# Performance work log

Measured on AMD Instinct MI355X. Metric: run time of the kernel, lower is better.

## Reference

```python
import jax, jax.numpy as jnp
import numpy as np

B, S, E, H = 2, 2048, 1024, 16
D = E // H

def setup_inputs() -> dict:
    key = jax.random.key(0)
    ks = jax.random.split(key, 5)
    return {
        "hidden_states": jax.random.normal(ks[0], (B, S, E), dtype=jnp.float32),
        "c_attn_w": jax.random.normal(ks[1], (E, 3 * E), dtype=jnp.float32) * 0.02,
        "c_attn_b": jax.random.normal(ks[2], (3 * E,), dtype=jnp.float32) * 0.02,
        "c_proj_w": jax.random.normal(ks[3], (E, E), dtype=jnp.float32) * 0.02,
        "c_proj_b": jax.random.normal(ks[4], (E,), dtype=jnp.float32) * 0.02,
    }

def reference(hidden_states, c_attn_w, c_attn_b, c_proj_w, c_proj_b):
    x = hidden_states                      # [B, S, E]
    b, s, _ = x.shape
    w_q, w_k, w_v = jnp.split(c_attn_w, 3, axis=1)   # each [E, E]
    q_b, k_b, v_b = jnp.split(c_attn_b, 3, axis=0)   # each [E]

    # value projection
    v = x @ w_v + v_b                                        # [B,S,E]
    v = v.reshape(b, s, H, D).transpose(0, 2, 1, 3)          # [B,H,S,D]

    # fused query: ((x Wq + qb) Wk^T + kb)
    q = (x @ w_q + q_b) @ w_k.T + k_b                        # [B,S,E]
    qh = q.reshape(b, s, H, D).transpose(0, 2, 1, 3)         # [B,H,S,D]

    # key side is RAW hidden states split per head
    kh = x.reshape(b, s, H, D).transpose(0, 2, 1, 3)         # [B,H,S,D]

    scale = 1.0 / jnp.float32(D) ** 0.5
    scores = jnp.einsum("bhqd,bhkd->bhqk",
                        qh.astype(jnp.float32),
                        kh.astype(jnp.float32)) * scale       # [B,H,S,S] fp32

    causal = jnp.tril(jnp.ones((s, s), dtype=bool))
    mask_value = jnp.finfo(jnp.float32).min
    scores = jnp.where(causal[None, None], scores, mask_value)

    probs = jax.nn.softmax(scores, axis=-1).astype(v.dtype)  # [B,H,S,S]

    out = jnp.einsum("bhqk,bhkd->bhqd", probs, v)            # [B,H,S,D]
    out = out.transpose(0, 2, 1, 3).reshape(b, s, E)         # [B,S,E]
    out = out @ c_proj_w + c_proj_b
    return out
```

## Files before the change

### kernel.cpp

```cpp
#include <hip/hip_runtime.h>

typedef __attribute__((ext_vector_type(8))) __bf16 bf16x8;
typedef __attribute__((ext_vector_type(4))) __bf16 bf16x4;
typedef __attribute__((ext_vector_type(4))) float f32x4;

typedef __attribute__((address_space(1))) void as1_void;
typedef __attribute__((address_space(3))) void as3_void;

__device__ __forceinline__ void gl_lds16(const void* g, void* l) {
    __builtin_amdgcn_global_load_lds((const as1_void*)g, (as3_void*)l, 16, 0, 0);
}

__device__ __forceinline__ const bf16x8* swz(const __bf16* base, int row, int chunk) {
    return (const bf16x8*)((const char*)base + row * 128 + ((chunk ^ (row & 7)) * 16));
}

#define QSCALE (0.125f * 1.44269504f)

__global__ __launch_bounds__(256) void prep_kernel(
    const float* __restrict__ x, const float* __restrict__ caw,
    const float* __restrict__ cpw,
    __bf16* __restrict__ xb, __bf16* __restrict__ wvt,
    __bf16* __restrict__ wpt, __bf16* __restrict__ wqt,
    __bf16* __restrict__ wkn)
{
    __shared__ float tile[32 * 33];
    int bid = blockIdx.x;
    int tid = threadIdx.x;
    if (bid < 1024) {
        int nt = bid >> 5, kt = bid & 31;
        int tx = tid & 31, ty = tid >> 5;
        int n0 = nt * 32, k0 = kt * 32;
#pragma unroll
        for (int i = 0; i < 4; ++i)
            tile[(ty + i * 8) * 33 + tx] = caw[(long)(k0 + ty + i * 8) * 3072 + 2048 + n0 + tx];
        __syncthreads();
#pragma unroll
        for (int i = 0; i < 4; ++i)
            wvt[(long)(n0 + ty + i * 8) * 1024 + k0 + tx] = (__bf16)tile[tx * 33 + ty + i * 8];
    } else if (bid < 2048) {
        int v = bid - 1024;
        int nt = v >> 5, kt = v & 31;
        int tx = tid & 31, ty = tid >> 5;
        int n0 = nt * 32, k0 = kt * 32;
#pragma unroll
        for (int i = 0; i < 4; ++i)
            tile[(ty + i * 8) * 33 + tx] = cpw[(long)(k0 + ty + i * 8) * 1024 + n0 + tx];
        __syncthreads();
#pragma unroll
        for (int i = 0; i < 4; ++i)
            wpt[(long)(n0 + ty + i * 8) * 1024 + k0 + tx] = (__bf16)tile[tx * 33 + ty + i * 8];
    } else if (bid < 3072) {
        int v = bid - 2048;
        int nt = v >> 5, kt = v & 31;
        int tx = tid & 31, ty = tid >> 5;
        int n0 = nt * 32, k0 = kt * 32;
#pragma unroll
        for (int i = 0; i < 4; ++i)
            tile[(ty + i * 8) * 33 + tx] = caw[(long)(k0 + ty + i * 8) * 3072 + n0 + tx];
        __syncthreads();
#pragma unroll
        for (int i = 0; i < 4; ++i)
            wqt[(long)(n0 + ty + i * 8) * 1024 + k0 + tx] = (__bf16)tile[tx * 33 + ty + i * 8];
    } else if (bid < 4096) {
        int e = (bid - 3072) * 1024 + tid * 4;
        int n = e >> 10, k = e & 1023;
        float4 f = *(const float4*)(caw + (long)n * 3072 + 1024 + k);
        bf16x4 o = {(__bf16)f.x, (__bf16)f.y, (__bf16)f.z, (__bf16)f.w};
        *(bf16x4*)(wkn + e) = o;
    } else {
        long e = (long)(bid - 4096) * 1024 + tid * 4;
        float4 f = *(const float4*)(x + e);
        bf16x4 o = {(__bf16)f.x, (__bf16)f.y, (__bf16)f.z, (__bf16)f.w};
        *(bf16x4*)(xb + e) = o;
    }
}

template <bool BF16OUT, int BN>
__global__ __launch_bounds__(256) void gemm_bt(
    const __bf16* __restrict__ A, int lda,
    const __bf16* __restrict__ B, int ldb,
    const float* __restrict__ bias,
    void* __restrict__ C, int ldc, int K, float oscale)
{
    constexpr int NT = BN / 32;
    __shared__ __bf16 As[128 * 64];
    __shared__ __bf16 Bs[BN * 64];
    const int tid = threadIdx.x;
    const int lane = tid & 63;
    const int wave = tid >> 6;
    const int quad = lane >> 4, l16 = lane & 15;
    const long m0 = (long)blockIdx.y * 128;
    const long n0 = (long)blockIdx.x * BN;
    const int wm = (wave >> 1) * 64, wn = (wave & 1) * (BN / 2);

    f32x4 acc[4][NT] = {};

    for (int k0 = 0; k0 < K; k0 += 64) {
#pragma unroll
        for (int c = tid; c < (128 + BN) * 8; c += 256) {
            int row = c >> 3, cc = (c & 7) ^ (row & 7);
            if (row < 128)
                gl_lds16(A + (m0 + row) * lda + k0 + cc * 8, As + c * 8);
            else
                gl_lds16(B + (n0 + row - 128) * ldb + k0 + cc * 8, Bs + (c - 1024) * 8);
        }
        __syncthreads();
#pragma unroll
        for (int kk = 0; kk < 2; ++kk) {
            bf16x8 af[4], bfr[NT];
#pragma unroll
            for (int i = 0; i < 4; ++i)
                af[i] = *swz(As, wm + i * 16 + l16, kk * 4 + quad);
#pragma unroll
            for (int j = 0; j < NT; ++j)
                bfr[j] = *swz(Bs, wn + j * 16 + l16, kk * 4 + quad);
#pragma unroll
            for (int i = 0; i < 4; ++i)
#pragma unroll
                for (int j = 0; j < NT; ++j)
                    acc[i][j] = __builtin_amdgcn_mfma_f32_16x16x32_bf16(af[i], bfr[j], acc[i][j], 0, 0, 0);
        }
        __syncthreads();
    }
#pragma unroll
    for (int i = 0; i < 4; ++i) {
        long row = m0 + wm + i * 16 + quad * 4;
#pragma unroll
        for (int j = 0; j < NT; ++j) {
            int col = (int)n0 + wn + j * 16 + l16;
            float bb = bias ? bias[col] : 0.f;
#pragma unroll
            for (int r = 0; r < 4; ++r) {
                float v = (acc[i][j][r] + bb) * oscale;
                if (BF16OUT)
                    ((__bf16*)C)[(row + r) * ldc + col] = (__bf16)v;
                else
                    ((float*)C)[(row + r) * ldc + col] = v;
            }
        }
    }
}

__global__ __launch_bounds__(256) void gemm_qv(
    const __bf16* __restrict__ Aq,
    const __bf16* __restrict__ Av,
    const __bf16* __restrict__ B,
    const float* __restrict__ bias,
    __bf16* __restrict__ Qout,
    __bf16* __restrict__ VTout)
{
    __shared__ __bf16 smem[128 * 136];
    __bf16* As = smem;
    __bf16* Bs = smem + 8192;
    const int tid = threadIdx.x;
    const int lane = tid & 63;
    const int wave = tid >> 6;
    const int quad = lane >> 4, l16 = lane & 15;
    const long m0 = (long)blockIdx.y * 128;
    const long n0 = (long)blockIdx.x * 128;
    const int wm = (wave >> 1) * 64, wn = (wave & 1) * 64;
    const __bf16* A = (n0 < 1024) ? Aq : Av;
    const float osc = (n0 < 1024) ? QSCALE : 1.0f;

    f32x4 acc[4][4] = {};

    for (int k0 = 0; k0 < 1024; k0 += 64) {
#pragma unroll
        for (int c = tid; c < 2048; c += 256) {
            int row = c >> 3, cc = (c & 7) ^ (row & 7);
            if (row < 128)
                gl_lds16(A + (m0 + row) * 1024 + k0 + cc * 8, As + c * 8);
            else
                gl_lds16(B + (n0 + row - 128) * 1024 + k0 + cc * 8, Bs + (c - 1024) * 8);
        }
        __syncthreads();
#pragma unroll
        for (int kk = 0; kk < 2; ++kk) {
            bf16x8 af[4], bfr[4];
#pragma unroll
            for (int i = 0; i < 4; ++i)
                af[i] = *swz(As, wm + i * 16 + l16, kk * 4 + quad);
#pragma unroll
            for (int j = 0; j < 4; ++j)
                bfr[j] = *swz(Bs, wn + j * 16 + l16, kk * 4 + quad);
#pragma unroll
            for (int i = 0; i < 4; ++i)
#pragma unroll
                for (int j = 0; j < 4; ++j)
                    acc[i][j] = __builtin_amdgcn_mfma_f32_16x16x32_bf16(af[i], bfr[j], acc[i][j], 0, 0, 0);
        }
        __syncthreads();
    }

    if (n0 < 1024) {
#pragma unroll
        for (int i = 0; i < 4; ++i) {
            long row = m0 + wm + i * 16 + quad * 4;
#pragma unroll
            for (int j = 0; j < 4; ++j) {
                int col = (int)n0 + wn + j * 16 + l16;
                float bb = bias[col];
#pragma unroll
                for (int r = 0; r < 4; ++r)
                    Qout[(row + r) * 1024 + col] = (__bf16)((acc[i][j][r] + bb) * osc);
            }
        }
    } else {
        __syncthreads();
#pragma unroll
        for (int i = 0; i < 4; ++i) {
#pragma unroll
            for (int j = 0; j < 4; ++j) {
                int col = (int)n0 + wn + j * 16 + l16;
                float bb = bias[col];
                bf16x4 v;
#pragma unroll
                for (int r = 0; r < 4; ++r) v[r] = (__bf16)(acc[i][j][r] + bb);
                *(bf16x4*)(smem + (wn + j * 16 + l16) * 136 + wm + i * 16 + quad * 4) = v;
            }
        }
        __syncthreads();
        const int d0 = (int)n0 - 1024;
        const int bb = (int)(m0 >> 11);
        const int sl = (int)(m0 & 2047);
#pragma unroll
        for (int pass = 0; pass < 16; ++pass) {
            int idx = pass * 256 + tid;
            int n = idx >> 5;
            int mc = (idx & 31) * 4;
            bf16x4 v = *(const bf16x4*)(smem + n * 136 + mc);
            *(bf16x4*)(VTout + ((long)(bb * 1024 + d0 + n)) * 2048 + sl + mc) = v;
        }
    }
}

__global__ __launch_bounds__(512) void attn_kernel(
    const __bf16* __restrict__ Q,
    const __bf16* __restrict__ Xb,
    const __bf16* __restrict__ VT,
    __bf16* __restrict__ O)
{
    __shared__ __bf16 Ks[2 * 8192];
    __shared__ __bf16 Vs[2 * 8192];
    __shared__ __bf16 Ps[8 * 1024];
    const int tid = threadIdx.x;
    const int lane = tid & 63;
    const int wave = tid >> 6;
    const int group = wave >> 2;
    const int w4 = wave & 3;
    const int quad = lane >> 4, l16 = lane & 15;
    const int qa = blockIdx.y;
    const int qb = 31 - qa;
    const int qt = group ? qb : qa;
    const int bh = blockIdx.x;
    const int b = bh >> 4, h = bh & 15;
    const long rowbase = (long)b * 2048;

    const int s0 = tid;
    const int c0 = ((s0 & 7) ^ ((s0 >> 3) & 7)) * 8;

    bf16x8 ones;
#pragma unroll
    for (int i = 0; i < 8; ++i) ones[i] = (__bf16)1.0f;

    bf16x8 qfr[2];
    {
        const __bf16* qp = Q + (rowbase + qt * 64 + w4 * 16 + l16) * 1024 + h * 64 + quad * 8;
        qfr[0] = *(const bf16x8*)(qp);
        qfr[1] = *(const bf16x8*)(qp + 32);
    }

    const __bf16* kp0 = Xb + (rowbase + (s0 >> 3)) * 1024 + h * 64 + c0;
    const __bf16* vp0 = VT + ((long)(b * 1024 + h * 64 + (s0 >> 3))) * 2048 + c0;

    auto stage_tile = [&](int j, int buf, int sub) {
        gl_lds16(kp0 + (long)j * 65536, Ks + buf * 8192 + sub * 4096 + s0 * 8);
        gl_lds16(vp0 + j * 64, Vs + buf * 8192 + sub * 4096 + s0 * 8);
    };
    stage_tile(0, 0, 0);
    stage_tile(1, 0, 1);

    const int nouter = (qb + 2) >> 1;

    f32x4 oacc[4] = {};
    f32x4 lacc = {};
    __bf16* Pw = Ps + wave * 1024;

    for (int jj = 0; jj < nouter; ++jj) {
        __syncthreads();
        if (jj + 1 < nouter) {
            stage_tile(2 * jj + 2, (jj + 1) & 1, 0);
            stage_tile(2 * jj + 3, (jj + 1) & 1, 1);
        }

#pragma unroll
        for (int sub = 0; sub < 2; ++sub) {
            const int j = 2 * jj + sub;
            if (j > qt) continue;
            const __bf16* Kb = Ks + (jj & 1) * 8192 + sub * 4096;
            const __bf16* Vb = Vs + (jj & 1) * 8192 + sub * 4096;

            bf16x8 kf[2][4], vf[2][4];
#pragma unroll
            for (int kk = 0; kk < 2; ++kk)
#pragma unroll
                for (int kt = 0; kt < 4; ++kt) {
                    kf[kk][kt] = *swz(Kb, kt * 16 + l16, kk * 4 + quad);
                    vf[kk][kt] = *swz(Vb, kt * 16 + l16, kk * 4 + quad);
                }

            f32x4 sacc[4] = {};
            __builtin_amdgcn_s_setprio(1);
#pragma unroll
            for (int kk = 0; kk < 2; ++kk)
#pragma unroll
                for (int kt = 0; kt < 4; ++kt)
                    sacc[kt] = __builtin_amdgcn_mfma_f32_16x16x32_bf16(
                        kf[kk][kt], qfr[kk], sacc[kt], 0, 0, 0);
            __builtin_amdgcn_s_setprio(0);

            if (j == qt) {
                const int qloc = w4 * 16 + l16;
#pragma unroll
                for (int kt = 0; kt < 4; ++kt) {
                    bf16x4 pk;
#pragma unroll
                    for (int r = 0; r < 4; ++r) {
                        float s = sacc[kt][r];
                        if (kt * 16 + quad * 4 + r > qloc) s = -1e30f;
                        pk[r] = (__bf16)exp2f(s);
                    }
                    *(bf16x4*)((char*)Pw + l16 * 128 +
                               (((kt * 2 + (quad >> 1)) ^ (l16 & 7)) * 16) + (quad & 1) * 8) = pk;
                }
            } else {
#pragma unroll
                for (int kt = 0; kt < 4; ++kt) {
                    bf16x4 pk;
#pragma unroll
                    for (int r = 0; r < 4; ++r)
                        pk[r] = (__bf16)exp2f(sacc[kt][r]);
                    *(bf16x4*)((char*)Pw + l16 * 128 +
                               (((kt * 2 + (quad >> 1)) ^ (l16 & 7)) * 16) + (quad & 1) * 8) = pk;
                }
            }

            __builtin_amdgcn_s_setprio(1);
#pragma unroll
            for (int kk = 0; kk < 2; ++kk) {
                bf16x8 pf = *swz(Pw, l16, kk * 4 + quad);
                lacc = __builtin_amdgcn_mfma_f32_16x16x32_bf16(ones, pf, lacc, 0, 0, 0);
#pragma unroll
                for (int dt = 0; dt < 4; ++dt)
                    oacc[dt] = __builtin_amdgcn_mfma_f32_16x16x32_bf16(
                        vf[kk][dt], pf, oacc[dt], 0, 0, 0);
            }
            __builtin_amdgcn_s_setprio(0);
        }
    }

    {
        float inv = 1.0f / lacc[0];
        long row = rowbase + qt * 64 + w4 * 16 + l16;
#pragma unroll
        for (int dt = 0; dt < 4; ++dt) {
            bf16x4 ov;
#pragma unroll
            for (int r = 0; r < 4; ++r) ov[r] = (__bf16)(oacc[dt][r] * inv);
            *(bf16x4*)(O + row * 1024 + h * 64 + dt * 16 + quad * 4) = ov;
        }
    }
}

extern "C" void kernel_launch(void* const* d_in, const int* in_sizes, int n_in,
                              void* d_out, int out_size, void* d_ws, size_t ws_size,
                              hipStream_t stream) {
    const float* x   = (const float*)d_in[0];
    const float* caw = (const float*)d_in[1];
    const float* cab = (const float*)d_in[2];
    const float* cpw = (const float*)d_in[3];
    const float* cpb = (const float*)d_in[4];

    char* p = (char*)d_ws;
    auto alloc = [&](size_t bytes) {
        void* r = (void*)p;
        p += (bytes + 255) & ~(size_t)255;
        return r;
    };
    __bf16* xb    = (__bf16*)alloc(4096UL * 1024 * 2);
    __bf16* wkn   = (__bf16*)alloc(1024UL * 1024 * 2);
    __bf16* wvt   = (__bf16*)alloc(1024UL * 1024 * 2);
    __bf16* wqt   = (__bf16*)alloc(1024UL * 1024 * 2);
    __bf16* wpt   = (__bf16*)alloc(1024UL * 1024 * 2);
    __bf16* tb    = (__bf16*)alloc(4096UL * 1024 * 2);
    __bf16* qbuf  = (__bf16*)alloc(4096UL * 1024 * 2);
    __bf16* vt    = (__bf16*)alloc(2048UL * 2048 * 2);

    prep_kernel<<<8192, 256, 0, stream>>>(x, caw, cpw, xb, wvt, wpt, wqt, wkn);
    gemm_bt<true, 64><<<dim3(16, 32), 256, 0, stream>>>(xb, 1024, wqt, 1024, cab,
                                                        (void*)tb, 1024, 1024, 1.0f);
    gemm_qv<<<dim3(16, 32), 256, 0, stream>>>(tb, xb, wkn, cab + 1024, qbuf, vt);
    attn_kernel<<<dim3(32, 16), 512, 0, stream>>>(qbuf, xb, vt, tb);
    gemm_bt<false, 64><<<dim3(16, 32), 256, 0, stream>>>(tb, 1024, wpt, 1024, cpb,
                                                         d_out, 1024, 1024, 1.0f);
    (void)in_sizes; (void)n_in; (void)out_size; (void)ws_size;
}
```

Before: 181.2 us.

## Split the long query tile's extra key tiles across both wave groups

In the attention kernel each block pairs a short query tile (qa) with a long one (qb), and the group handling qa used to sit idle once its causal range ended. Key tiles beyond qa are now split between both groups: each group computes half of the 64-key scores and P·V for the qb tile. Group 0's partial output and row sum are combined with group 1's through LDS at the end. This balances work between the two groups at the cost of extra barriers, more registers for a second accumulator set, and a reduction step.

```diff
diff --git a/kernel.cpp b/kernel.cpp
--- a/kernel.cpp
+++ b/kernel.cpp
@@ -161,7 +161,6 @@
     const long n0 = (long)blockIdx.x * 128;
     const int wm = (wave >> 1) * 64, wn = (wave & 1) * 64;
     const __bf16* A = (n0 < 1024) ? Aq : Av;
-    const float osc = (n0 < 1024) ? QSCALE : 1.0f;
 
     f32x4 acc[4][4] = {};
 
@@ -203,7 +202,7 @@
                 float bb = bias[col];
 #pragma unroll
                 for (int r = 0; r < 4; ++r)
-                    Qout[(row + r) * 1024 + col] = (__bf16)((acc[i][j][r] + bb) * osc);
+                    Qout[(row + r) * 1024 + col] = (__bf16)((acc[i][j][r] + bb) * QSCALE);
             }
         }
     } else {
@@ -264,11 +263,14 @@
 #pragma unroll
     for (int i = 0; i < 8; ++i) ones[i] = (__bf16)1.0f;
 
-    bf16x8 qfr[2];
+    bf16x8 qfa[2], qfb[2];
     {
-        const __bf16* qp = Q + (rowbase + qt * 64 + w4 * 16 + l16) * 1024 + h * 64 + quad * 8;
-        qfr[0] = *(const bf16x8*)(qp);
-        qfr[1] = *(const bf16x8*)(qp + 32);
+        const __bf16* qpa = Q + (rowbase + qa * 64 + w4 * 16 + l16) * 1024 + h * 64 + quad * 8;
+        const __bf16* qpb = Q + (rowbase + qb * 64 + w4 * 16 + l16) * 1024 + h * 64 + quad * 8;
+        qfa[0] = *(const bf16x8*)(qpa);
+        qfa[1] = *(const bf16x8*)(qpa + 32);
+        qfb[0] = *(const bf16x8*)(qpb);
+        qfb[1] = *(const bf16x8*)(qpb + 32);
     }
 
     const __bf16* kp0 = Xb + (rowbase + (s0 >> 3)) * 1024 + h * 64 + c0;
@@ -284,8 +286,10 @@
     const int nouter = (qb + 2) >> 1;
 
     f32x4 oacc[4] = {};
-    f32x4 lacc = {};
-    __bf16* Pw = Ps + wave * 1024;
+    f32x4 oacch[4] = {};
+    f32x4 lacc = {}, lacch = {};
+    __bf16* Pown = Ps + wave * 1024;
+    __bf16* Pspl = Ps + w4 * 1024;
 
     for (int jj = 0; jj < nouter; ++jj) {
         __syncthreads();
@@ -297,69 +301,148 @@
 #pragma unroll
         for (int sub = 0; sub < 2; ++sub) {
             const int j = 2 * jj + sub;
-            if (j > qt) continue;
+            if (sub == 1 && 2 * jj == qa) __syncthreads();
+            if (j > qb) continue;
             const __bf16* Kb = Ks + (jj & 1) * 8192 + sub * 4096;
             const __bf16* Vb = Vs + (jj & 1) * 8192 + sub * 4096;
 
-            bf16x8 kf[2][4], vf[2][4];
-#pragma unroll
-            for (int kk = 0; kk < 2; ++kk)
-#pragma unroll
-                for (int kt = 0; kt < 4; ++kt) {
-                    kf[kk][kt] = *swz(Kb, kt * 16 + l16, kk * 4 + quad);
-                    vf[kk][kt] = *swz(Vb, kt * 16 + l16, kk * 4 + quad);
+            if (j <= qa) {
+                bf16x8 kf[2][4], vf[2][4];
+#pragma unroll
+                for (int kk = 0; kk < 2; ++kk)
+#pragma unroll
+                    for (int kt = 0; kt < 4; ++kt) {
+                        kf[kk][kt] = *swz(Kb, kt * 16 + l16, kk * 4 + quad);
+                        vf[kk][kt] = *swz(Vb, kt * 16 + l16, kk * 4 + quad);
+                    }
+
+                f32x4 sacc[4] = {};
+                __builtin_amdgcn_s_setprio(1);
+#pragma unroll
+                for (int kk = 0; kk < 2; ++kk) {
+                    bf16x8 qf = group ? qfb[kk] : qfa[kk];
+#pragma unroll
+                    for (int kt = 0; kt < 4; ++kt)
+                        sacc[kt] = __builtin_amdgcn_mfma_f32_16x16x32_bf16(
+                            kf[kk][kt], qf, sacc[kt], 0, 0, 0);
                 }
-
-            f32x4 sacc[4] = {};
-            __builtin_amdgcn_s_setprio(1);
-#pragma unroll
-            for (int kk = 0; kk < 2; ++kk)
-#pragma unroll
-                for (int kt = 0; kt < 4; ++kt)
-                    sacc[kt] = __builtin_amdgcn_mfma_f32_16x16x32_bf16(
-                        kf[kk][kt], qfr[kk], sacc[kt], 0, 0, 0);
-            __builtin_amdgcn_s_setprio(0);
-
-            if (j == qt) {
+                __builtin_amdgcn_s_setprio(0);
+
+                if (j == qt) {
+                    const int qloc = w4 * 16 + l16;
+#pragma unroll
+                    for (int kt = 0; kt < 4; ++kt) {
+                        bf16x4 pk;
+#pragma unroll
+                        for (int r = 0; r < 4; ++r) {
+                            float s = sacc[kt][r];
+                            if (kt * 16 + quad * 4 + r > qloc) s = -1e30f;
+                            pk[r] = (__bf16)exp2f(s);
+                        }
+                        *(bf16x4*)((char*)Pown + l16 * 128 +
+                                   (((kt * 2 + (quad >> 1)) ^ (l16 & 7)) * 16) + (quad & 1) * 8) = pk;
+                    }
+                } else {
+#pragma unroll
+                    for (int kt = 0; kt < 4; ++kt) {
+                        bf16x4 pk;
+#pragma unroll
+                        for (int r = 0; r < 4; ++r)
+                            pk[r] = (__bf16)exp2f(sacc[kt][r]);
+                        *(bf16x4*)((char*)Pown + l16 * 128 +
+                                   (((kt * 2 + (quad >> 1)) ^ (l16 & 7)) * 16) + (quad & 1) * 8) = pk;
+                    }
+                }
+
+                __builtin_amdgcn_s_setprio(1);
+#pragma unroll
+                for (int kk = 0; kk < 2; ++kk) {
+                    bf16x8 pf = *swz(Pown, l16, kk * 4 + quad);
+                    lacc = __builtin_amdgcn_mfma_f32_16x16x32_bf16(ones, pf, lacc, 0, 0, 0);
+#pragma unroll
+                    for (int dt = 0; dt < 4; ++dt)
+                        oacc[dt] = __builtin_amdgcn_mfma_f32_16x16x32_bf16(
+                            vf[kk][dt], pf, oacc[dt], 0, 0, 0);
+                }
+                __builtin_amdgcn_s_setprio(0);
+            } else {
+                const int ktb = group * 2;
+                bf16x8 kf2[2][2], vf2[4];
+#pragma unroll
+                for (int kk = 0; kk < 2; ++kk)
+#pragma unroll
+                    for (int t = 0; t < 2; ++t)
+                        kf2[kk][t] = *swz(Kb, (ktb + t) * 16 + l16, kk * 4 + quad);
+#pragma unroll
+                for (int dt = 0; dt < 4; ++dt)
+                    vf2[dt] = *swz(Vb, dt * 16 + l16, group * 4 + quad);
+
+                f32x4 s2[2] = {};
+                __builtin_amdgcn_s_setprio(1);
+#pragma unroll
+                for (int kk = 0; kk < 2; ++kk)
+#pragma unroll
+                    for (int t = 0; t < 2; ++t)
+                        s2[t] = __builtin_amdgcn_mfma_f32_16x16x32_bf16(
+                            kf2[kk][t], qfb[kk], s2[t], 0, 0, 0);
+                __builtin_amdgcn_s_setprio(0);
+
                 const int qloc = w4 * 16 + l16;
-#pragma unroll
-                for (int kt = 0; kt < 4; ++kt) {
+                const bool diag = (j == qb);
+#pragma unroll
+                for (int t = 0; t < 2; ++t) {
+                    const int kt = ktb + t;
                     bf16x4 pk;
 #pragma unroll
                     for (int r = 0; r < 4; ++r) {
-                        float s = sacc[kt][r];
-                        if (kt * 16 + quad * 4 + r > qloc) s = -1e30f;
+                        float s = s2[t][r];
+                        if (diag && kt * 16 + quad * 4 + r > qloc) s = -1e30f;
                         pk[r] = (__bf16)exp2f(s);
                     }
-                    *(bf16x4*)((char*)Pw + l16 * 128 +
+                    *(bf16x4*)((char*)Pspl + l16 * 128 +
                                (((kt * 2 + (quad >> 1)) ^ (l16 & 7)) * 16) + (quad & 1) * 8) = pk;
                 }
-            } else {
-#pragma unroll
-                for (int kt = 0; kt < 4; ++kt) {
-                    bf16x4 pk;
-#pragma unroll
-                    for (int r = 0; r < 4; ++r)
-                        pk[r] = (__bf16)exp2f(sacc[kt][r]);
-                    *(bf16x4*)((char*)Pw + l16 * 128 +
-                               (((kt * 2 + (quad >> 1)) ^ (l16 & 7)) * 16) + (quad & 1) * 8) = pk;
+
+                __builtin_amdgcn_s_setprio(1);
+                bf16x8 pf = *swz(Pspl, l16, group * 4 + quad);
+                if (group) {
+                    lacc = __builtin_amdgcn_mfma_f32_16x16x32_bf16(ones, pf, lacc, 0, 0, 0);
+#pragma unroll
+                    for (int dt = 0; dt < 4; ++dt)
+                        oacc[dt] = __builtin_amdgcn_mfma_f32_16x16x32_bf16(
+                            vf2[dt], pf, oacc[dt], 0, 0, 0);
+                } else {
+                    lacch = __builtin_amdgcn_mfma_f32_16x16x32_bf16(ones, pf, lacch, 0, 0, 0);
+#pragma unroll
+                    for (int dt = 0; dt < 4; ++dt)
+                        oacch[dt] = __builtin_amdgcn_mfma_f32_16x16x32_bf16(
+                            vf2[dt], pf, oacch[dt], 0, 0, 0);
                 }
+                __builtin_amdgcn_s_setprio(0);
             }
-
-            __builtin_amdgcn_s_setprio(1);
-#pragma unroll
-            for (int kk = 0; kk < 2; ++kk) {
-                bf16x8 pf = *swz(Pw, l16, kk * 4 + quad);
-                lacc = __builtin_amdgcn_mfma_f32_16x16x32_bf16(ones, pf, lacc, 0, 0, 0);
-#pragma unroll
-                for (int dt = 0; dt < 4; ++dt)
-                    oacc[dt] = __builtin_amdgcn_mfma_f32_16x16x32_bf16(
-                        vf[kk][dt], pf, oacc[dt], 0, 0, 0);
-            }
-            __builtin_amdgcn_s_setprio(0);
-        }
-    }
-
+        }
+    }
+
+    __syncthreads();
+    float* xch = (float*)Ks;
+    if (!group) {
+        const int base = (w4 * 64 + lane) * 20;
+#pragma unroll
+        for (int dt = 0; dt < 4; ++dt)
+            *(f32x4*)(xch + base + dt * 4) = oacch[dt];
+        xch[base + 16] = lacch[0];
+    }
+    __syncthreads();
+    if (group) {
+        const int base = (w4 * 64 + lane) * 20;
+#pragma unroll
+        for (int dt = 0; dt < 4; ++dt) {
+            f32x4 part = *(const f32x4*)(xch + base + dt * 4);
+#pragma unroll
+            for (int r = 0; r < 4; ++r) oacc[dt][r] += part[r];
+        }
+        lacc[0] += xch[base + 16];
+    }
     {
         float inv = 1.0f / lacc[0];
         long row = rowbase + qt * 64 + w4 * 16 + l16;
```

Result: slower. 196.2 us (+8.3%).

## Fuse Q projection into attention kernel and merge T/V projection GEMMs

Applied to the files above, without the earlier changes.

The second-stage Q projection (T·Wk^T) moves into the attention kernel. Each block computes its own 128 Q rows for one head from T and the head's Wk slice, staged through the K/V shared buffers, then places them in registers. The T and V projection GEMMs now share one launch with a flat block index, which removes a kernel launch and the Q buffer round trip through global memory. In exchange the attention kernel does a serial K=1024 GEMM prologue with no overlap. Each T row tile is also reloaded by all 16 heads, and the V GEMM now sits on the critical path alongside T.

```diff
diff --git a/kernel.cpp b/kernel.cpp
--- a/kernel.cpp
+++ b/kernel.cpp
@@ -76,144 +76,110 @@
     }
 }
 
-template <bool BF16OUT, int BN>
-__global__ __launch_bounds__(256) void gemm_bt(
-    const __bf16* __restrict__ A, int lda,
-    const __bf16* __restrict__ B, int ldb,
-    const float* __restrict__ bias,
-    void* __restrict__ C, int ldc, int K, float oscale)
+__global__ __launch_bounds__(256) void gemm_tv(
+    const __bf16* __restrict__ xb, const __bf16* __restrict__ wqt,
+    const __bf16* __restrict__ wvt, const float* __restrict__ cab,
+    __bf16* __restrict__ tb, __bf16* __restrict__ vt)
 {
-    constexpr int NT = BN / 32;
-    __shared__ __bf16 As[128 * 64];
-    __shared__ __bf16 Bs[BN * 64];
+    __shared__ __bf16 smem[128 * 136];
+    const int bid = blockIdx.x;
     const int tid = threadIdx.x;
     const int lane = tid & 63;
     const int wave = tid >> 6;
     const int quad = lane >> 4, l16 = lane & 15;
-    const long m0 = (long)blockIdx.y * 128;
-    const long n0 = (long)blockIdx.x * BN;
-    const int wm = (wave >> 1) * 64, wn = (wave & 1) * (BN / 2);
-
-    f32x4 acc[4][NT] = {};
-
-    for (int k0 = 0; k0 < K; k0 += 64) {
-#pragma unroll
-        for (int c = tid; c < (128 + BN) * 8; c += 256) {
-            int row = c >> 3, cc = (c & 7) ^ (row & 7);
-            if (row < 128)
-                gl_lds16(A + (m0 + row) * lda + k0 + cc * 8, As + c * 8);
-            else
-                gl_lds16(B + (n0 + row - 128) * ldb + k0 + cc * 8, Bs + (c - 1024) * 8);
-        }
-        __syncthreads();
-#pragma unroll
-        for (int kk = 0; kk < 2; ++kk) {
-            bf16x8 af[4], bfr[NT];
-#pragma unroll
-            for (int i = 0; i < 4; ++i)
-                af[i] = *swz(As, wm + i * 16 + l16, kk * 4 + quad);
-#pragma unroll
-            for (int j = 0; j < NT; ++j)
-                bfr[j] = *swz(Bs, wn + j * 16 + l16, kk * 4 + quad);
-#pragma unroll
-            for (int i = 0; i < 4; ++i)
-#pragma unroll
-                for (int j = 0; j < NT; ++j)
-                    acc[i][j] = __builtin_amdgcn_mfma_f32_16x16x32_bf16(af[i], bfr[j], acc[i][j], 0, 0, 0);
-        }
-        __syncthreads();
-    }
-#pragma unroll
-    for (int i = 0; i < 4; ++i) {
-        long row = m0 + wm + i * 16 + quad * 4;
-#pragma unroll
-        for (int j = 0; j < NT; ++j) {
-            int col = (int)n0 + wn + j * 16 + l16;
-            float bb = bias ? bias[col] : 0.f;
-#pragma unroll
-            for (int r = 0; r < 4; ++r) {
-                float v = (acc[i][j][r] + bb) * oscale;
-                if (BF16OUT)
-                    ((__bf16*)C)[(row + r) * ldc + col] = (__bf16)v;
+
+    if (bid < 512) {
+        __bf16* As = smem;
+        __bf16* Bs = smem + 8192;
+        const int bx = bid & 15, by = bid >> 4;
+        const long m0 = (long)by * 128;
+        const long n0 = (long)bx * 64;
+        const int wm = (wave >> 1) * 64, wn = (wave & 1) * 32;
+
+        f32x4 acc[4][2] = {};
+        for (int k0 = 0; k0 < 1024; k0 += 64) {
+#pragma unroll
+            for (int c = tid; c < 1536; c += 256) {
+                int row = c >> 3, cc = (c & 7) ^ (row & 7);
+                if (row < 128)
+                    gl_lds16(xb + (m0 + row) * 1024 + k0 + cc * 8, As + c * 8);
                 else
-                    ((float*)C)[(row + r) * ldc + col] = v;
-            }
-        }
-    }
-}
-
-__global__ __launch_bounds__(256) void gemm_qv(
-    const __bf16* __restrict__ Aq,
-    const __bf16* __restrict__ Av,
-    const __bf16* __restrict__ B,
-    const float* __restrict__ bias,
-    __bf16* __restrict__ Qout,
-    __bf16* __restrict__ VTout)
-{
-    __shared__ __bf16 smem[128 * 136];
-    __bf16* As = smem;
-    __bf16* Bs = smem + 8192;
-    const int tid = threadIdx.x;
-    const int lane = tid & 63;
-    const int wave = tid >> 6;
-    const int quad = lane >> 4, l16 = lane & 15;
-    const long m0 = (long)blockIdx.y * 128;
-    const long n0 = (long)blockIdx.x * 128;
-    const int wm = (wave >> 1) * 64, wn = (wave & 1) * 64;
-    const __bf16* A = (n0 < 1024) ? Aq : Av;
-    const float osc = (n0 < 1024) ? QSCALE : 1.0f;
-
-    f32x4 acc[4][4] = {};
-
-    for (int k0 = 0; k0 < 1024; k0 += 64) {
-#pragma unroll
-        for (int c = tid; c < 2048; c += 256) {
-            int row = c >> 3, cc = (c & 7) ^ (row & 7);
-            if (row < 128)
-                gl_lds16(A + (m0 + row) * 1024 + k0 + cc * 8, As + c * 8);
-            else
-                gl_lds16(B + (n0 + row - 128) * 1024 + k0 + cc * 8, Bs + (c - 1024) * 8);
-        }
-        __syncthreads();
-#pragma unroll
-        for (int kk = 0; kk < 2; ++kk) {
-            bf16x8 af[4], bfr[4];
-#pragma unroll
-            for (int i = 0; i < 4; ++i)
-                af[i] = *swz(As, wm + i * 16 + l16, kk * 4 + quad);
-#pragma unroll
-            for (int j = 0; j < 4; ++j)
-                bfr[j] = *swz(Bs, wn + j * 16 + l16, kk * 4 + quad);
-#pragma unroll
-            for (int i = 0; i < 4; ++i)
-#pragma unroll
-                for (int j = 0; j < 4; ++j)
-                    acc[i][j] = __builtin_amdgcn_mfma_f32_16x16x32_bf16(af[i], bfr[j], acc[i][j], 0, 0, 0);
-        }
-        __syncthreads();
-    }
-
-    if (n0 < 1024) {
+                    gl_lds16(wqt + (n0 + row - 128) * 1024 + k0 + cc * 8, Bs + (c - 1024) * 8);
+            }
+            __syncthreads();
+#pragma unroll
+            for (int kk = 0; kk < 2; ++kk) {
+                bf16x8 af[4], bfr[2];
+#pragma unroll
+                for (int i = 0; i < 4; ++i)
+                    af[i] = *swz(As, wm + i * 16 + l16, kk * 4 + quad);
+#pragma unroll
+                for (int j = 0; j < 2; ++j)
+                    bfr[j] = *swz(Bs, wn + j * 16 + l16, kk * 4 + quad);
+#pragma unroll
+                for (int i = 0; i < 4; ++i)
+#pragma unroll
+                    for (int j = 0; j < 2; ++j)
+                        acc[i][j] = __builtin_amdgcn_mfma_f32_16x16x32_bf16(af[i], bfr[j], acc[i][j], 0, 0, 0);
+            }
+            __syncthreads();
+        }
 #pragma unroll
         for (int i = 0; i < 4; ++i) {
             long row = m0 + wm + i * 16 + quad * 4;
 #pragma unroll
+            for (int j = 0; j < 2; ++j) {
+                int col = (int)n0 + wn + j * 16 + l16;
+                float bb = cab[col];
+#pragma unroll
+                for (int r = 0; r < 4; ++r)
+                    tb[(row + r) * 1024 + col] = (__bf16)(acc[i][j][r] + bb);
+            }
+        }
+    } else {
+        __bf16* As = smem;
+        __bf16* Bs = smem + 8192;
+        const int v2 = bid - 512;
+        const int bx = v2 & 7, by = v2 >> 3;
+        const long m0 = (long)by * 128;
+        const long n0 = (long)bx * 128;
+        const int wm = (wave >> 1) * 64, wn = (wave & 1) * 64;
+
+        f32x4 acc[4][4] = {};
+        for (int k0 = 0; k0 < 1024; k0 += 64) {
+#pragma unroll
+            for (int c = tid; c < 2048; c += 256) {
+                int row = c >> 3, cc = (c & 7) ^ (row & 7);
+                if (row < 128)
+                    gl_lds16(xb + (m0 + row) * 1024 + k0 + cc * 8, As + c * 8);
+                else
+                    gl_lds16(wvt + (n0 + row - 128) * 1024 + k0 + cc * 8, Bs + (c - 1024) * 8);
+            }
+            __syncthreads();
+#pragma unroll
+            for (int kk = 0; kk < 2; ++kk) {
+                bf16x8 af[4], bfr[4];
+#pragma unroll
+                for (int i = 0; i < 4; ++i)
+                    af[i] = *swz(As, wm + i * 16 + l16, kk * 4 + quad);
+#pragma unroll
+                for (int j = 0; j < 4; ++j)
+                    bfr[j] = *swz(Bs, wn + j * 16 + l16, kk * 4 + quad);
+#pragma unroll
+                for (int i = 0; i < 4; ++i)
+#pragma unroll
+                    for (int j = 0; j < 4; ++j)
+                        acc[i][j] = __builtin_amdgcn_mfma_f32_16x16x32_bf16(af[i], bfr[j], acc[i][j], 0, 0, 0);
+            }
+            __syncthreads();
+        }
+        __syncthreads();
+#pragma unroll
+        for (int i = 0; i < 4; ++i) {
+#pragma unroll
             for (int j = 0; j < 4; ++j) {
                 int col = (int)n0 + wn + j * 16 + l16;
-                float bb = bias[col];
-#pragma unroll
-                for (int r = 0; r < 4; ++r)
-                    Qout[(row + r) * 1024 + col] = (__bf16)((acc[i][j][r] + bb) * osc);
-            }
-        }
-    } else {
-        __syncthreads();
-#pragma unroll
-        for (int i = 0; i < 4; ++i) {
-#pragma unroll
-            for (int j = 0; j < 4; ++j) {
-                int col = (int)n0 + wn + j * 16 + l16;
-                float bb = bias[col];
+                float bb = cab[2048 + col];
                 bf16x4 v;
 #pragma unroll
                 for (int r = 0; r < 4; ++r) v[r] = (__bf16)(acc[i][j][r] + bb);
@@ -221,8 +187,7 @@
             }
         }
         __syncthreads();
-        const int d0 = (int)n0 - 1024;
-        const int bb = (int)(m0 >> 11);
+        const int bb2 = (int)(m0 >> 11);
         const int sl = (int)(m0 & 2047);
 #pragma unroll
         for (int pass = 0; pass < 16; ++pass) {
@@ -230,15 +195,17 @@
             int n = idx >> 5;
             int mc = (idx & 31) * 4;
             bf16x4 v = *(const bf16x4*)(smem + n * 136 + mc);
-            *(bf16x4*)(VTout + ((long)(bb * 1024 + d0 + n)) * 2048 + sl + mc) = v;
+            *(bf16x4*)(vt + ((long)(bb2 * 1024 + (int)n0 + n)) * 2048 + sl + mc) = v;
         }
     }
 }
 
 __global__ __launch_bounds__(512) void attn_kernel(
-    const __bf16* __restrict__ Q,
+    const __bf16* __restrict__ T,
     const __bf16* __restrict__ Xb,
     const __bf16* __restrict__ VT,
+    const __bf16* __restrict__ WK,
+    const float* __restrict__ cab,
     __bf16* __restrict__ O)
 {
     __shared__ __bf16 Ks[2 * 8192];
@@ -266,9 +233,49 @@
 
     bf16x8 qfr[2];
     {
-        const __bf16* qp = Q + (rowbase + qt * 64 + w4 * 16 + l16) * 1024 + h * 64 + quad * 8;
-        qfr[0] = *(const bf16x8*)(qp);
-        qfr[1] = *(const bf16x8*)(qp + 32);
+        f32x4 qacc[4] = {};
+        for (int k0 = 0; k0 < 1024; k0 += 64) {
+#pragma unroll
+            for (int u = 0; u < 3; ++u) {
+                int c = tid + u * 512;
+                if (c < 1024) {
+                    int lr = c >> 3;
+                    int cc = (c & 7) ^ (lr & 7);
+                    int grow = (lr < 64) ? qa * 64 + lr : qb * 64 + (lr - 64);
+                    gl_lds16(T + (rowbase + grow) * 1024 + k0 + cc * 8, Ks + c * 8);
+                } else {
+                    int w = c - 1024;
+                    int lr = w >> 3;
+                    int cc = (w & 7) ^ (lr & 7);
+                    gl_lds16(WK + (long)(h * 64 + lr) * 1024 + k0 + cc * 8, Vs + w * 8);
+                }
+            }
+            __syncthreads();
+#pragma unroll
+            for (int kk = 0; kk < 2; ++kk) {
+                bf16x8 af = *swz(Ks + group * 4096, w4 * 16 + l16, kk * 4 + quad);
+#pragma unroll
+                for (int dt = 0; dt < 4; ++dt) {
+                    bf16x8 bfr = *swz(Vs, dt * 16 + l16, kk * 4 + quad);
+                    qacc[dt] = __builtin_amdgcn_mfma_f32_16x16x32_bf16(af, bfr, qacc[dt], 0, 0, 0);
+                }
+            }
+            __syncthreads();
+        }
+#pragma unroll
+        for (int dt = 0; dt < 4; ++dt) {
+            int d = dt * 16 + l16;
+            float bb = cab[1024 + h * 64 + d];
+#pragma unroll
+            for (int r = 0; r < 4; ++r) {
+                int row = group * 64 + w4 * 16 + quad * 4 + r;
+                float v = (qacc[dt][r] + bb) * QSCALE;
+                *(__bf16*)((char*)Ps + row * 128 + (((d >> 3) ^ (row & 7)) * 16) + (d & 7) * 2) = (__bf16)v;
+            }
+        }
+        __syncthreads();
+        qfr[0] = *swz(Ps + group * 4096, w4 * 16 + l16, quad);
+        qfr[1] = *swz(Ps + group * 4096, w4 * 16 + l16, 4 + quad);
     }
 
     const __bf16* kp0 = Xb + (rowbase + (s0 >> 3)) * 1024 + h * 64 + c0;
@@ -369,6 +376,63 @@
 #pragma unroll
             for (int r = 0; r < 4; ++r) ov[r] = (__bf16)(oacc[dt][r] * inv);
             *(bf16x4*)(O + row * 1024 + h * 64 + dt * 16 + quad * 4) = ov;
+        }
+    }
+}
+
+__global__ __launch_bounds__(256) void gemm_proj(
+    const __bf16* __restrict__ A, const __bf16* __restrict__ B,
+    const float* __restrict__ bias, float* __restrict__ C)
+{
+    __shared__ __bf16 As[128 * 64];
+    __shared__ __bf16 Bs[64 * 64];
+    const int tid = threadIdx.x;
+    const int lane = tid & 63;
+    const int wave = tid >> 6;
+    const int quad = lane >> 4, l16 = lane & 15;
+    const long m0 = (long)blockIdx.y * 128;
+    const long n0 = (long)blockIdx.x * 64;
+    const int wm = (wave >> 1) * 64, wn = (wave & 1) * 32;
+
+    f32x4 acc[4][2] = {};
+
+    for (int k0 = 0; k0 < 1024; k0 += 64) {
+#pragma unroll
+        for (int c = tid; c < 1536; c += 256) {
+            int row = c >> 3, cc = (c & 7) ^ (row & 7);
+            if (row < 128)
+                gl_lds16(A + (m0 + row) * 1024 + k0 + cc * 8, As + c * 8);
+            else
+                gl_lds16(B + (n0 + row - 128) * 1024 + k0 + cc * 8, Bs + (c - 1024) * 8);
+        }
+        __syncthreads();
+#pragma unroll
+        for (int kk = 0; kk < 2; ++kk) {
+            bf16x8 af[4], bfr[2];
+#pragma unroll
+            for (int i = 0; i < 4; ++i)
+                af[i] = *swz(As, wm + i * 16 + l16, kk * 4 + quad);
+#pragma unroll
+            for (int j = 0; j < 2; ++j)
+                bfr[j] = *swz(Bs, wn + j * 16 + l16, kk * 4 + quad);
+#pragma unroll
+            for (int i = 0; i < 4; ++i)
+#pragma unroll
+                for (int j = 0; j < 2; ++j)
+                    acc[i][j] = __builtin_amdgcn_mfma_f32_16x16x32_bf16(af[i], bfr[j], acc[i][j], 0, 0, 0);
+        }
+        __syncthreads();
+    }
+#pragma unroll
+    for (int i = 0; i < 4; ++i) {
+        long row = m0 + wm + i * 16 + quad * 4;
+#pragma unroll
+        for (int j = 0; j < 2; ++j) {
+            int col = (int)n0 + wn + j * 16 + l16;
+            float bb = bias[col];
+#pragma unroll
+            for (int r = 0; r < 4; ++r)
+                C[(row + r) * 1024 + col] = acc[i][j][r] + bb;
         }
     }
 }
@@ -394,15 +458,12 @@
     __bf16* wqt   = (__bf16*)alloc(1024UL * 1024 * 2);
     __bf16* wpt   = (__bf16*)alloc(1024UL * 1024 * 2);
     __bf16* tb    = (__bf16*)alloc(4096UL * 1024 * 2);
-    __bf16* qbuf  = (__bf16*)alloc(4096UL * 1024 * 2);
+    __bf16* abuf  = (__bf16*)alloc(4096UL * 1024 * 2);
     __bf16* vt    = (__bf16*)alloc(2048UL * 2048 * 2);
 
     prep_kernel<<<8192, 256, 0, stream>>>(x, caw, cpw, xb, wvt, wpt, wqt, wkn);
-    gemm_bt<true, 64><<<dim3(16, 32), 256, 0, stream>>>(xb, 1024, wqt, 1024, cab,
-                                                        (void*)tb, 1024, 1024, 1.0f);
-    gemm_qv<<<dim3(16, 32), 256, 0, stream>>>(tb, xb, wkn, cab + 1024, qbuf, vt);
-    attn_kernel<<<dim3(32, 16), 512, 0, stream>>>(qbuf, xb, vt, tb);
-    gemm_bt<false, 64><<<dim3(16, 32), 256, 0, stream>>>(tb, 1024, wpt, 1024, cpb,
-                                                         d_out, 1024, 1024, 1.0f);
+    gemm_tv<<<768, 256, 0, stream>>>(xb, wqt, wvt, cab, tb, vt);
+    attn_kernel<<<dim3(32, 16), 512, 0, stream>>>(tb, xb, vt, wkn, cab, abuf);
+    gemm_proj<<<dim3(16, 32), 256, 0, stream>>>(abuf, wpt, cpb, (float*)d_out);
     (void)in_sizes; (void)n_in; (void)out_size; (void)ws_size;
 }
```

New measurement: 174.9 us. -3.5%, faster.
